# Optimization experiments

Hardware: AMD Instinct MI355X
Metric: run time of the kernel (lower is better)

## Reference

```python
import jax, jax.numpy as jnp
import numpy as np

B, N, OUTERDIM, DIM, N_CLASSES = 2, 6000, 1024, 512, 2
HEADS, DIM_HEAD, INNER = 8, 64, 512
LANDMARKS, PINV_ITERS, KPAD = 256, 6, 16  # residual conv kernel 33 -> pad 16
SCALE = DIM_HEAD ** -0.5


def layer_norm(x, g, b, eps=1e-5):
    mu = x.mean(-1, keepdims=True)
    var = jnp.var(x, axis=-1, keepdims=True)
    return (x - mu) * jax.lax.rsqrt(var + eps) * g + b


def moore_penrose_pinv(x, iters=PINV_ITERS):
    # x: [b, h, m, m]
    abs_x = jnp.abs(x)
    col = abs_x.sum(-1)
    row = abs_x.sum(-2)
    z = jnp.swapaxes(x, -1, -2) / (jnp.max(col) * jnp.max(row))
    I = jnp.eye(x.shape[-1], dtype=x.dtype)
    for _ in range(iters):
        xz = x @ z
        z = 0.25 * z @ (13 * I - xz @ (15 * I - xz @ (7 * I - xz)))
    return z


def nystrom_attention(x, w_qkv, w_out, b_out, conv_w):
    b, n, _ = x.shape
    pad = (-n) % LANDMARKS
    xp = jnp.pad(x, ((0, 0), (pad, 0), (0, 0)))  # pad at FRONT, as in lucidrains impl
    npad = n + pad
    qkv = xp @ w_qkv.T  # [b, npad, 3*inner]
    q, k, v = [t.reshape(b, npad, HEADS, DIM_HEAD).transpose(0, 2, 1, 3)
               for t in jnp.split(qkv, 3, axis=-1)]
    q = q * SCALE
    l = npad // LANDMARKS  # tokens per landmark
    q_l = q.reshape(b, HEADS, LANDMARKS, l, DIM_HEAD).sum(3) / l
    k_l = k.reshape(b, HEADS, LANDMARKS, l, DIM_HEAD).sum(3) / l
    attn1 = jax.nn.softmax(jnp.einsum('bhid,bhjd->bhij', q, k_l), axis=-1)   # [b,h,npad,m]
    attn2 = jax.nn.softmax(jnp.einsum('bhid,bhjd->bhij', q_l, k_l), axis=-1)  # [b,h,m,m]
    attn3 = jax.nn.softmax(jnp.einsum('bhid,bhjd->bhij', q_l, k), axis=-1)    # [b,h,m,npad]
    out = (attn1 @ moore_penrose_pinv(attn2)) @ (attn3 @ v)  # [b,h,npad,d]
    # depthwise residual conv over sequence dim (per head), kernel (33,1)
    out = out + jax.lax.conv_general_dilated(
        v, conv_w, window_strides=(1, 1), padding=((KPAD, KPAD), (0, 0)),
        dimension_numbers=('NCHW', 'OIHW', 'NCHW'), feature_group_count=HEADS)
    out = out.transpose(0, 2, 1, 3).reshape(b, npad, INNER)
    out = out @ w_out.T + b_out
    return out[:, -n:]


def setup_inputs() -> dict:
    key = jax.random.key(0)
    ks = jax.random.split(key, 12)
    w = lambda k, shape: 0.02 * jax.random.normal(k, shape, dtype=jnp.float32)
    inp = {
        'data': jax.random.normal(ks[0], (B, N, OUTERDIM), dtype=jnp.float32),
        'w1': w(ks[1], (DIM, OUTERDIM)), 'b1': jnp.zeros((DIM,), jnp.float32),
        'cls_token': jax.random.normal(ks[2], (1, 1, DIM), dtype=jnp.float32),
        'ln1_g': jnp.ones((DIM,), jnp.float32), 'ln1_b': jnp.zeros((DIM,), jnp.float32),
        'qkv1_w': w(ks[3], (3 * INNER, DIM)),
        'out1_w': w(ks[4], (DIM, INNER)), 'out1_b': jnp.zeros((DIM,), jnp.float32),
        'conv1_w': w(ks[5], (HEADS, 1, 33, 1)),
        'ln2_g': jnp.ones((DIM,), jnp.float32), 'ln2_b': jnp.zeros((DIM,), jnp.float32),
        'qkv2_w': w(ks[6], (3 * INNER, DIM)),
        'out2_w': w(ks[7], (DIM, INNER)), 'out2_b': jnp.zeros((DIM,), jnp.float32),
        'conv2_w': w(ks[8], (HEADS, 1, 33, 1)),
        'lnf_g': jnp.ones((DIM,), jnp.float32), 'lnf_b': jnp.zeros((DIM,), jnp.float32),
        'w2': w(ks[9], (N_CLASSES, DIM)), 'b2': jnp.zeros((N_CLASSES,), jnp.float32),
    }
    return inp


def reference(data, w1, b1, cls_token, ln1_g, ln1_b, qkv1_w, out1_w, out1_b, conv1_w,
              ln2_g, ln2_b, qkv2_w, out2_w, out2_b, conv2_w, lnf_g, lnf_b, w2, b2):
    h = jax.nn.relu(data @ w1.T + b1)  # [B, N, DIM]
    H = h.shape[1]
    side = int(np.ceil(np.sqrt(H)))
    add = side * side - H
    h = jnp.concatenate([h, h[:, :add]], axis=1)  # square padding: 6084
    cls = jnp.broadcast_to(cls_token, (h.shape[0], 1, h.shape[2]))
    h = jnp.concatenate([cls, h], axis=1)  # +CLS: 6085
    h = h + nystrom_attention(layer_norm(h, ln1_g, ln1_b), qkv1_w, out1_w, out1_b, conv1_w)
    h = h + nystrom_attention(layer_norm(h, ln2_g, ln2_b), qkv2_w, out2_w, out2_b, conv2_w)
    h = layer_norm(h, lnf_g, lnf_b)[:, 0]
    logits = h @ w2.T + b2
    return logits
```

## Files before the change

### kernel.cpp

```cpp
#include <hip/hip_runtime.h>
#include <cstdint>
#include <cstddef>

namespace {

constexpr int DIMC  = 512;
constexpr int SEQ   = 6085;
constexpr int NPAD  = 6144;
constexpr int PADF  = 59;
constexpr int LMK   = 256;
constexpr int BHN   = 16;
constexpr int KSPL  = 16;
constexpr int MPADR = 6016;

typedef __attribute__((ext_vector_type(8))) short bf8_t;
typedef __attribute__((ext_vector_type(4))) float f4_t;

#define MFMA(a, b, c) __builtin_amdgcn_mfma_f32_16x16x32_bf16(a, b, c, 0, 0, 0)

#define SWZB(r, cu) (((((r) << 6) + ((cu) << 1))) ^ (((r) & 7) << 4))

#define GLDS16(gp, lp) __builtin_amdgcn_global_load_lds( \
    (const __attribute__((address_space(1))) void*)(gp), \
    (__attribute__((address_space(3))) void*)(lp), 16, 0, 0)

__device__ __forceinline__ ushort f2bf(float f) {
    union { float f; uint32_t u; } c{f};
    uint32_t u = c.u;
    return (ushort)((u + 0x7FFFu + ((u >> 16) & 1u)) >> 16);
}
__device__ __forceinline__ float bf2f(ushort u) {
    union { uint32_t u; float f; } c{(uint32_t)u << 16};
    return c.f;
}

__device__ __forceinline__ float waveSum(float v) {
#pragma unroll
    for (int o = 32; o > 0; o >>= 1) v += __shfl_xor(v, o, 64);
    return v;
}
__device__ __forceinline__ float waveMax(float v) {
#pragma unroll
    for (int o = 32; o > 0; o >>= 1) v = fmaxf(v, __shfl_xor(v, o, 64));
    return v;
}
__device__ __forceinline__ float blockSum256(float v, float* sm) {
    v = waveSum(v);
    __syncthreads();
    if ((threadIdx.x & 63) == 0) sm[threadIdx.x >> 6] = v;
    __syncthreads();
    return sm[0] + sm[1] + sm[2] + sm[3];
}
__device__ __forceinline__ float blockMax256(float v, float* sm) {
    v = waveMax(v);
    __syncthreads();
    if ((threadIdx.x & 63) == 0) sm[threadIdx.x >> 6] = v;
    __syncthreads();
    return fmaxf(fmaxf(sm[0], sm[1]), fmaxf(sm[2], sm[3]));
}
__device__ __forceinline__ float grpMax(float v) {
    v = fmaxf(v, __shfl_xor(v, 1, 64));
    v = fmaxf(v, __shfl_xor(v, 2, 64));
    v = fmaxf(v, __shfl_xor(v, 4, 64));
    v = fmaxf(v, __shfl_xor(v, 8, 64));
    return v;
}
__device__ __forceinline__ float grpSum(float v) {
    v += __shfl_xor(v, 1, 64);
    v += __shfl_xor(v, 2, 64);
    v += __shfl_xor(v, 4, 64);
    v += __shfl_xor(v, 8, 64);
    return v;
}

template<int EPI>
__global__ __launch_bounds__(256)
void gemm_bt(const ushort* __restrict__ A, const ushort* __restrict__ B,
             void* __restrict__ Cv, int M, int N, int K,
             int lda, int ldb, int ldc,
             long long sA, long long sB, long long sC,
             const float* __restrict__ bias, int relu,
             ushort* __restrict__ qp, ushort* __restrict__ kp, ushort* __restrict__ vp)
{
    __shared__ __align__(16) char As_s[128 * 128];
    __shared__ __align__(16) char Bs_s[128 * 128];
    const int gx = gridDim.x, gy = gridDim.y;
    const int total = gx * gy * gridDim.z;
    int flat = (blockIdx.z * gy + blockIdx.y) * gx + blockIdx.x;
    {
        int q = total >> 3, r = total & 7;
        int xcd = flat & 7, idx = flat >> 3;
        flat = (xcd < r ? xcd * (q + 1) : r * (q + 1) + (xcd - r) * q) + idx;
    }
    const int z = flat / (gx * gy);
    const int rem = flat - z * gx * gy;
    const int by = rem / gx, bx = rem - by * gx;

    const ushort* Ab = A + (size_t)z * sA;
    const ushort* Bb = B + (size_t)z * sB;
    const int row0 = by * 128, col0 = bx * 128;
    const int tid = threadIdx.x, wid = tid >> 6, lane = tid & 63;
    const int wr = wid >> 1, wc = wid & 1, lr = lane & 15, kg = lane >> 4;
    const int srow = lane >> 3, sq = lane & 7;
    f4_t acc[4][4] = {};
    for (int k0 = 0; k0 < K; k0 += 64) {
        __syncthreads();
#pragma unroll
        for (int i = 0; i < 4; ++i) {
            int r = wid * 32 + i * 8 + srow;
            int qs = sq ^ (r & 7);
            GLDS16(Ab + (size_t)(row0 + r) * lda + k0 + qs * 8,
                   As_s + (wid * 32 + i * 8) * 128);
        }
#pragma unroll
        for (int i = 0; i < 4; ++i) {
            int r = wid * 32 + i * 8 + srow;
            int qs = sq ^ (r & 7);
            GLDS16(Bb + (size_t)(col0 + r) * ldb + k0 + qs * 8,
                   Bs_s + (wid * 32 + i * 8) * 128);
        }
        asm volatile("s_waitcnt vmcnt(0)" ::: "memory");
        __syncthreads();
#pragma unroll
        for (int ks = 0; ks < 2; ++ks) {
            bf8_t af[4], bg[4];
#pragma unroll
            for (int mr = 0; mr < 4; ++mr) {
                int r = wr * 64 + mr * 16 + lr;
                af[mr] = *(const bf8_t*)(As_s + r * 128 + ((((ks << 2) | kg) ^ (r & 7)) << 4));
            }
#pragma unroll
            for (int nr = 0; nr < 4; ++nr) {
                int r = wc * 64 + nr * 16 + lr;
                bg[nr] = *(const bf8_t*)(Bs_s + r * 128 + ((((ks << 2) | kg) ^ (r & 7)) << 4));
            }
#pragma unroll
            for (int mr = 0; mr < 4; ++mr)
#pragma unroll
                for (int nr = 0; nr < 4; ++nr)
                    acc[mr][nr] = MFMA(af[mr], bg[nr], acc[mr][nr]);
        }
    }
#pragma unroll
    for (int mr = 0; mr < 4; ++mr) {
#pragma unroll
        for (int nr = 0; nr < 4; ++nr) {
#pragma unroll
            for (int r = 0; r < 4; ++r) {
                int gm = row0 + wr * 64 + mr * 16 + kg * 4 + r;
                int gn = col0 + wc * 64 + nr * 16 + lr;
                if (gm >= M || gn >= N) continue;
                float val = acc[mr][nr][r];
                if (EPI == 0) {
                    if (bias) val += bias[gn];
                    if (relu) val = fmaxf(val, 0.f);
                    ((float*)Cv)[(size_t)z * sC + (size_t)gm * ldc + gn] = val;
                } else if (EPI == 1) {
                    ((ushort*)Cv)[(size_t)z * sC + (size_t)gm * ldc + gn] = f2bf(val);
                } else {
                    int b = (gm >= NPAD) ? 1 : 0;
                    int i = gm - b * NPAD;
                    int which = gn >> 9, hh = (gn >> 6) & 7, d = gn & 63;
                    int bh = b * 8 + hh;
                    if (which == 0)
                        qp[((size_t)bh * NPAD + i) * 64 + d] = f2bf(val * 0.125f);
                    else if (which == 1)
                        kp[((size_t)bh * NPAD + i) * 64 + d] = f2bf(val);
                    else
                        vp[((size_t)bh * NPAD + i) * 64 + d] = f2bf(val);
                }
            }
        }
    }
}

__global__ __launch_bounds__(256)
void gemm_ns(const ushort* __restrict__ A, const ushort* __restrict__ B,
             ushort* __restrict__ C, ushort* __restrict__ C2, ushort* __restrict__ CT,
             float alpha, float c2d, int K, int N,
             long long sA, long long sB, long long sC, long long sCT)
{
    __shared__ __align__(16) char As_s[64 * 64];
    __shared__ __align__(16) char Bs_s[64 * 64];
    const int z = blockIdx.z;
    const int row0 = blockIdx.y * 64, col0 = blockIdx.x * 64;
    const int tid = threadIdx.x;
    const int wid = tid >> 6, lane = tid & 63;
    const int lr = lane & 15, kg = lane >> 4;
    const ushort* Ab = A + (size_t)z * sA;
    const ushort* Bb = B + (size_t)z * sB;
    f4_t acc[4] = {};
    const int am = tid >> 2, ac8 = (tid & 3) * 8;
    for (int k0 = 0; k0 < K; k0 += 32) {
        *(bf8_t*)(As_s + SWZB(am, ac8)) = *(const bf8_t*)&Ab[(size_t)(row0 + am) * K + k0 + ac8];
#pragma unroll
        for (int p = 0; p < 8; ++p) {
            int kk = p * 4 + (tid >> 6), n = tid & 63;
            *(ushort*)(Bs_s + SWZB(n, kk)) = Bb[(size_t)(k0 + kk) * N + col0 + n];
        }
        __syncthreads();
        bf8_t af = *(const bf8_t*)(As_s + SWZB(wid * 16 + lr, kg * 8));
#pragma unroll
        for (int j = 0; j < 4; ++j) {
            bf8_t bg = *(const bf8_t*)(Bs_s + SWZB(j * 16 + lr, kg * 8));
            acc[j] = MFMA(af, bg, acc[j]);
        }
        __syncthreads();
    }
#pragma unroll
    for (int j = 0; j < 4; ++j) {
#pragma unroll
        for (int r = 0; r < 4; ++r) {
            int gm = row0 + wid * 16 + kg * 4 + r;
            int gn = col0 + j * 16 + lr;
            float val = alpha * acc[j][r];
            if (C)  C[(size_t)z * sC + (size_t)gm * N + gn] = f2bf(val);
            if (C2) C2[(size_t)z * sC + (size_t)gm * N + gn] = f2bf(((gm == gn) ? c2d : 0.f) - val);
            if (CT) CT[(size_t)z * sCT + (size_t)gn * LMK + gm] = f2bf(val);
        }
    }
}

__global__ __launch_bounds__(256)
void pv_splitk(const ushort* __restrict__ S, const ushort* __restrict__ v,
               float* __restrict__ o2p)
{
    __shared__ __align__(16) char As_s[128 * 64];
    __shared__ __align__(16) char Bs_s[64 * 64];
    const int split = blockIdx.x, mt = blockIdx.y, bh = blockIdx.z;
    const int tid = threadIdx.x;
    const int wid = tid >> 6, lane = tid & 63;
    const int lr = lane & 15, kg = lane >> 4;
    const ushort* Sb = S + (size_t)bh * LMK * NPAD + (size_t)(mt * 128) * NPAD;
    const ushort* vb = v + (size_t)bh * NPAD * 64;
    const int ks0 = split * (NPAD / KSPL);
    f4_t acc[2][4] = {};
    for (int k0 = ks0; k0 < ks0 + NPAD / KSPL; k0 += 32) {
#pragma unroll
        for (int p = 0; p < 2; ++p) {
            int idx = p * 256 + tid;
            int m = idx >> 2, kc = (idx & 3) * 8;
            *(bf8_t*)(As_s + SWZB(m, kc)) = *(const bf8_t*)&Sb[(size_t)m * NPAD + k0 + kc];
        }
#pragma unroll
        for (int p = 0; p < 8; ++p) {
            int kk = p * 4 + (tid >> 6), n = tid & 63;
            *(ushort*)(Bs_s + SWZB(n, kk)) = vb[(size_t)(k0 + kk) * 64 + n];
        }
        __syncthreads();
        bf8_t af[2], bg[4];
#pragma unroll
        for (int i = 0; i < 2; ++i)
            af[i] = *(const bf8_t*)(As_s + SWZB(wid * 32 + i * 16 + lr, kg * 8));
#pragma unroll
        for (int j = 0; j < 4; ++j)
            bg[j] = *(const bf8_t*)(Bs_s + SWZB(j * 16 + lr, kg * 8));
#pragma unroll
        for (int i = 0; i < 2; ++i)
#pragma unroll
            for (int j = 0; j < 4; ++j)
                acc[i][j] = MFMA(af[i], bg[j], acc[i][j]);
        __syncthreads();
    }
#pragma unroll
    for (int i = 0; i < 2; ++i)
#pragma unroll
        for (int j = 0; j < 4; ++j)
#pragma unroll
            for (int r = 0; r < 4; ++r) {
                int gm = mt * 128 + wid * 32 + i * 16 + kg * 4 + r;
                int gn = j * 16 + lr;
                o2p[((size_t)(split * BHN + bh) * LMK + gm) * 64 + gn] = acc[i][j][r];
            }
}

__global__ void reduce_o2(const float* __restrict__ o2p, ushort* __restrict__ o2) {
    int idx = blockIdx.x * 256 + threadIdx.x;
    int bh = idx >> 14, e = idx & 16383;
    float s = 0.f;
#pragma unroll
    for (int sp = 0; sp < KSPL; ++sp)
        s += o2p[((size_t)(sp * BHN + bh) << 14) + e];
    o2[idx] = f2bf(s);
}

__global__ __launch_bounds__(256)
void attn1_fused(const ushort* __restrict__ q, const ushort* __restrict__ kl,
                 const ushort* __restrict__ Wt, ushort* __restrict__ ot)
{
    __shared__ __align__(16) char P_s[64 * 512];
    const int mt = blockIdx.x;
    const int bh = blockIdx.y;
    const int b = bh >> 3, hh = bh & 7;
    const int tid = threadIdx.x, wid = tid >> 6, lane = tid & 63;
    const int lr = lane & 15, kg = lane >> 4;
    const int row0 = mt * 64, rowb = wid * 16;
    const ushort* qb  = q  + (size_t)bh * NPAD * 64;
    const ushort* klb = kl + (size_t)bh * LMK * 64;
    const ushort* Wtb = Wt + (size_t)bh * 128 * 256;

    f4_t acc[16];
#pragma unroll
    for (int nf = 0; nf < 16; ++nf) acc[nf] = (f4_t){0.f, 0.f, 0.f, 0.f};
#pragma unroll
    for (int ks = 0; ks < 2; ++ks) {
        bf8_t af = *(const bf8_t*)&qb[(size_t)(row0 + rowb + lr) * 64 + ks * 32 + kg * 8];
#pragma unroll
        for (int nf = 0; nf < 16; ++nf) {
            bf8_t bg = *(const bf8_t*)&klb[(size_t)(nf * 16 + lr) * 64 + ks * 32 + kg * 8];
            acc[nf] = MFMA(af, bg, acc[nf]);
        }
    }
    float inv_s[4];
    {
        float mx[4] = {-3.0e38f, -3.0e38f, -3.0e38f, -3.0e38f};
#pragma unroll
        for (int nf = 0; nf < 16; ++nf)
#pragma unroll
            for (int r = 0; r < 4; ++r) mx[r] = fmaxf(mx[r], acc[nf][r]);
#pragma unroll
        for (int r = 0; r < 4; ++r) mx[r] = grpMax(mx[r]);
        float sum[4] = {0.f, 0.f, 0.f, 0.f};
        const int rb2 = rowb + kg * 4;
        const int cc2 = (lr & 7) * 2, chi = lr >> 3;
#pragma unroll
        for (int nf = 0; nf < 16; ++nf)
#pragma unroll
            for (int r = 0; r < 4; ++r) {
                float e = __expf(acc[nf][r] - mx[r]);
                sum[r] += e;
                int row = rb2 + r;
                int chunk = (2 * nf + chi) ^ (row & 7);
                *(ushort*)(P_s + row * 512 + chunk * 16 + cc2) = f2bf(e);
            }
#pragma unroll
        for (int r = 0; r < 4; ++r) inv_s[r] = 1.f / grpSum(sum[r]);
    }
    f4_t acc2[4] = {};
#pragma unroll
    for (int kt = 0; kt < 8; ++kt) {
        int row = rowb + lr;
        int chunk = (kt * 4 + kg) ^ (row & 7);
        bf8_t af2 = *(const bf8_t*)(P_s + row * 512 + chunk * 16);
#pragma unroll
        for (int nf = 0; nf < 4; ++nf) {
            bf8_t bg = *(const bf8_t*)&Wtb[(size_t)(nf * 16 + lr) * 256 + kt * 32 + kg * 8];
            acc2[nf] = MFMA(af2, bg, acc2[nf]);
        }
    }
#pragma unroll
    for (int nf = 0; nf < 4; ++nf)
#pragma unroll
        for (int r = 0; r < 4; ++r) {
            int gm = row0 + rowb + kg * 4 + r;
            int gn = nf * 16 + lr;
            ot[((size_t)(b * NPAD + gm)) * DIMC + hh * 64 + gn] = f2bf(acc2[nf][r] * inv_s[r]);
        }
}

__global__ void cvt_bf16(const float* __restrict__ in, ushort* __restrict__ out, int n8) {
    int i = blockIdx.x * 256 + threadIdx.x;
    if (i >= n8) return;
    float4 a = ((const float4*)in)[i * 2], b = ((const float4*)in)[i * 2 + 1];
    ushort4 lo = { f2bf(a.x), f2bf(a.y), f2bf(a.z), f2bf(a.w) };
    ushort4 hi = { f2bf(b.x), f2bf(b.y), f2bf(b.z), f2bf(b.w) };
    ((ushort4*)out)[i * 2] = lo;
    ((ushort4*)out)[i * 2 + 1] = hi;
}

__global__ void extend_h(float* __restrict__ h, const float* __restrict__ cls) {
    int b = blockIdx.y, bx = blockIdx.x;
    float* hb = h + (size_t)b * SEQ * DIMC;
    for (int c = threadIdx.x; c < DIMC; c += 256) {
        if (bx == 0) hb[c] = cls[c];
        else hb[(size_t)(6000 + bx) * DIMC + c] = hb[(size_t)bx * DIMC + c];
    }
}

__global__ void zero_xp_pad(ushort* __restrict__ xp) {
    int e = blockIdx.x * 256 + threadIdx.x;
    int b = e / (PADF * DIMC);
    int rest = e - b * (PADF * DIMC);
    xp[(size_t)b * NPAD * DIMC + rest] = 0;
}

__global__ __launch_bounds__(128)
void ln_to_xp(const float* __restrict__ h, const float* __restrict__ g,
              const float* __restrict__ bb, ushort* __restrict__ xp)
{
    __shared__ float sm[2];
    int r = blockIdx.x;
    int b = r / SEQ, i = r - b * SEQ;
    int t = threadIdx.x;
    const float4* row = (const float4*)(h + (size_t)r * DIMC);
    float4 x = row[t];
    float s  = x.x + x.y + x.z + x.w;
    float sq = x.x * x.x + x.y * x.y + x.z * x.z + x.w * x.w;
    s = waveSum(s);
    sq = waveSum(sq);
    int w = t >> 6;
    if ((t & 63) == 0) sm[w] = s;
    __syncthreads();
    float S = sm[0] + sm[1];
    __syncthreads();
    if ((t & 63) == 0) sm[w] = sq;
    __syncthreads();
    float SQ = sm[0] + sm[1];
    float mu = S * (1.f / DIMC);
    float var = SQ * (1.f / DIMC) - mu * mu;
    float rs = rsqrtf(var + 1e-5f);
    float4 gg = ((const float4*)g)[t];
    float4 bv = ((const float4*)bb)[t];
    ushort4 o;
    o.x = f2bf((x.x - mu) * rs * gg.x + bv.x);
    o.y = f2bf((x.y - mu) * rs * gg.y + bv.y);
    o.z = f2bf((x.z - mu) * rs * gg.z + bv.z);
    o.w = f2bf((x.w - mu) * rs * gg.w + bv.w);
    ((ushort4*)(xp + ((size_t)b * NPAD + PADF + i) * DIMC))[t] = o;
}

__global__ void landmark_mean(const ushort* __restrict__ in, ushort* __restrict__ out) {
    int m = blockIdx.x, bh = blockIdx.y, d = threadIdx.x;
    const ushort* p = in + ((size_t)bh * NPAD + (size_t)m * (NPAD / LMK)) * 64 + d;
    float s = 0.f;
#pragma unroll
    for (int j = 0; j < NPAD / LMK; ++j) s += bf2f(p[(size_t)j * 64]);
    out[((size_t)bh * LMK + m) * 64 + d] = f2bf(s * (1.f / (NPAD / LMK)));
}

__global__ __launch_bounds__(256)
void softmax_bf_wide(ushort* __restrict__ S) {
    __shared__ float sm[4];
    ushort* p = S + (size_t)blockIdx.x * NPAD;
    int t = threadIdx.x;
    float v[24];
    float mx = -1e30f;
#pragma unroll
    for (int j = 0; j < 24; ++j) { v[j] = bf2f(p[j * 256 + t]); mx = fmaxf(mx, v[j]); }
    float bm = blockMax256(mx, sm);
    float s = 0.f;
#pragma unroll
    for (int j = 0; j < 24; ++j) { v[j] = __expf(v[j] - bm); s += v[j]; }
    float bs = blockSum256(s, sm);
    float inv = 1.f / bs;
#pragma unroll
    for (int j = 0; j < 24; ++j) p[j * 256 + t] = f2bf(v[j] * inv);
}

__global__ __launch_bounds__(256)
void softmax_bf256(ushort* __restrict__ S) {
    __shared__ float sm[4];
    ushort* p = S + (size_t)blockIdx.x * 256;
    int t = threadIdx.x;
    float v = bf2f(p[t]);
    float bm = blockMax256(v, sm);
    float e = __expf(v - bm);
    float bs = blockSum256(e, sm);
    p[t] = f2bf(e / bs);
}

__global__ __launch_bounds__(256)
void colsum_max(const ushort* __restrict__ X, float* __restrict__ scal) {
    __shared__ float sm[4];
    int bh = blockIdx.x, t = threadIdx.x;
    const ushort* Xb = X + ((size_t)bh << 16);
    float s = 0.f;
#pragma unroll 8
    for (int i = 0; i < 256; ++i) s += bf2f(Xb[(size_t)i * 256 + t]);
    float m = blockMax256(s, sm);
    if (t == 0) atomicMax((unsigned int*)scal, __float_as_uint(m));
}

__global__ void init_z(const ushort* __restrict__ X, const float* __restrict__ scal,
                       ushort* __restrict__ Z) {
    size_t e = (size_t)blockIdx.x * 256 + threadIdx.x;
    int c = (int)(e & 255);
    int r = (int)((e >> 8) & 255);
    size_t bh = e >> 16;
    float inv = 1.f / scal[0];
    Z[e] = f2bf(bf2f(X[(bh << 16) + (size_t)c * 256 + r]) * inv);
}

__global__ __launch_bounds__(256)
void conv_add(const ushort* __restrict__ v, const float* __restrict__ cw,
              ushort* __restrict__ ot)
{
    __shared__ float w[33];
    __shared__ ushort vt[96][64];
    int bh = blockIdx.y;
    int b = bh >> 3, hh = bh & 7;
    int i0 = blockIdx.x * 64;
    int t = threadIdx.x;
    if (t < 33) w[t] = cw[hh * 33 + t];
    const ushort* vb = v + (size_t)bh * NPAD * 64;
    int d = t & 63;
    for (int rr = t >> 6; rr < 96; rr += 4) {
        int j = i0 - 16 + rr;
        vt[rr][d] = (j >= 0 && j < NPAD) ? vb[(size_t)j * 64 + d] : (ushort)0;
    }
    __syncthreads();
    for (int ii = t >> 6; ii < 64; ii += 4) {
        float acc = 0.f;
#pragma unroll
        for (int kk = 0; kk < 33; ++kk) acc += w[kk] * bf2f(vt[ii + kk][d]);
        size_t off = ((size_t)(b * NPAD + i0 + ii)) * DIMC + hh * 64 + d;
        ot[off] = f2bf(bf2f(ot[off]) + acc);
    }
}

__global__ void residual_add(float* __restrict__ h, const float* __restrict__ y) {
    size_t e = (size_t)blockIdx.x * 256 + threadIdx.x;
    int c = (int)(e & 511);
    size_t ri = e >> 9;
    int i = (int)(ri % SEQ);
    int b = (int)(ri / SEQ);
    h[e] += y[((size_t)b * NPAD + PADF + i) * DIMC + c];
}

__global__ __launch_bounds__(256)
void final_head(const float* __restrict__ h, const float* __restrict__ g,
                const float* __restrict__ bb, const float* __restrict__ w2,
                const float* __restrict__ b2, float* __restrict__ out)
{
    __shared__ float row[DIMC];
    __shared__ float sm[4];
    int b = blockIdx.x;
    int t = threadIdx.x;
    const float* x = h + (size_t)b * SEQ * DIMC;
    float v0 = x[t], v1 = x[t + 256];
    float S = blockSum256(v0 + v1, sm);
    float SQ = blockSum256(v0 * v0 + v1 * v1, sm);
    float mu = S * (1.f / DIMC);
    float rs = rsqrtf(SQ * (1.f / DIMC) - mu * mu + 1e-5f);
    row[t] = (v0 - mu) * rs * g[t] + bb[t];
    row[t + 256] = (v1 - mu) * rs * g[t + 256] + bb[t + 256];
    __syncthreads();
    if (t < 64) {
        float a0 = 0.f, a1 = 0.f;
        for (int idx = t; idx < DIMC; idx += 64) {
            a0 += row[idx] * w2[idx];
            a1 += row[idx] * w2[DIMC + idx];
        }
        a0 = waveSum(a0);
        a1 = waveSum(a1);
        if (t == 0) {
            out[b * 2 + 0] = a0 + b2[0];
            out[b * 2 + 1] = a1 + b2[1];
        }
    }
}

void bt(int epi, const ushort* A, const ushort* B, void* C, int M, int N, int K,
        int lda, int ldb, int ldc, long long sA, long long sB, long long sC, int batch,
        const float* bias, int relu, ushort* qp, ushort* kp, ushort* vp, hipStream_t s)
{
    dim3 g((N + 127) / 128, (M + 127) / 128, batch), blk(256);
    switch (epi) {
    case 0: gemm_bt<0><<<g, blk, 0, s>>>(A, B, C, M, N, K, lda, ldb, ldc, sA, sB, sC, bias, relu, qp, kp, vp); break;
    case 1: gemm_bt<1><<<g, blk, 0, s>>>(A, B, C, M, N, K, lda, ldb, ldc, sA, sB, sC, bias, relu, qp, kp, vp); break;
    default: gemm_bt<2><<<g, blk, 0, s>>>(A, B, C, M, N, K, lda, ldb, ldc, sA, sB, sC, bias, relu, qp, kp, vp); break;
    }
}

void ns(const ushort* A, const ushort* B, ushort* C, ushort* C2, ushort* CT,
        float alpha, float c2d, int M, int N, int K,
        long long sA, long long sB, long long sC, long long sCT, hipStream_t s)
{
    dim3 g(N / 64, M / 64, BHN), blk(256);
    gemm_ns<<<g, blk, 0, s>>>(A, B, C, C2, CT, alpha, c2d, K, N, sA, sB, sC, sCT);
}

struct WS {
    float *h, *scal, *o2p, *y;
    ushort *xp, *q, *k, *v, *ql, *kl;
    ushort *datab, *w1b, *qkvwb1, *qkvwb2, *outwb1, *outwb2;
    ushort *X, *Z0, *Z1, *XZ, *TA, *TB, *TC;
    ushort *o2b, *Wt, *S, *ot;
};

void nystrom_layer(float* h, const float* lng, const float* lnb,
                   const ushort* qkvwb, const ushort* outwb, const float* outb,
                   const float* convw, const WS& w, hipStream_t s)
{
    const long long SM = (long long)LMK * LMK;
    zero_xp_pad<<<(2 * PADF * DIMC) / 256, 256, 0, s>>>(w.xp);
    ln_to_xp<<<2 * SEQ, 128, 0, s>>>(h, lng, lnb, w.xp);
    bt(2, w.xp, qkvwb, nullptr, 2 * NPAD, 3 * DIMC, DIMC, DIMC, DIMC, 0,
       0, 0, 0, 1, nullptr, 0, w.q, w.k, w.v, s);
    landmark_mean<<<dim3(LMK, BHN), 64, 0, s>>>(w.q, w.ql);
    landmark_mean<<<dim3(LMK, BHN), 64, 0, s>>>(w.k, w.kl);
    bt(1, w.ql, w.kl, w.X, LMK, LMK, 64, 64, 64, LMK,
       (long long)LMK * 64, (long long)LMK * 64, SM, BHN,
       nullptr, 0, nullptr, nullptr, nullptr, s);
    softmax_bf256<<<BHN * LMK, 256, 0, s>>>(w.X);
    hipMemsetAsync(w.scal, 0, 8, s);
    colsum_max<<<BHN, 256, 0, s>>>(w.X, w.scal);
    init_z<<<(BHN * LMK * LMK) / 256, 256, 0, s>>>(w.X, w.scal, w.Z0);
    ushort* Zc = w.Z0;
    ushort* Zn = w.Z1;
    for (int it = 0; it < 6; ++it) {
        ns(w.X, Zc, w.XZ, w.TA, nullptr, 1.f, 7.f, LMK, LMK, LMK, SM, SM, SM, 0, s);
        ns(w.XZ, w.TA, w.TB, w.TC, nullptr, 1.f, 15.f, LMK, LMK, LMK, SM, SM, SM, 0, s);
        ns(w.XZ, w.TC, w.TB, w.TA, nullptr, 1.f, 13.f, LMK, LMK, LMK, SM, SM, SM, 0, s);
        ns(Zc, w.TA, Zn, nullptr, nullptr, 0.25f, 0.f, LMK, LMK, LMK, SM, SM, SM, 0, s);
        ushort* t = Zc; Zc = Zn; Zn = t;
    }
    bt(1, w.ql, w.k, w.S, LMK, NPAD, 64, 64, 64, NPAD,
       (long long)LMK * 64, (long long)NPAD * 64, (long long)LMK * NPAD, BHN,
       nullptr, 0, nullptr, nullptr, nullptr, s);
    softmax_bf_wide<<<BHN * LMK, 256, 0, s>>>(w.S);
    pv_splitk<<<dim3(KSPL, 2, BHN), 256, 0, s>>>(w.S, w.v, w.o2p);
    reduce_o2<<<BHN * LMK * 64 / 256, 256, 0, s>>>(w.o2p, w.o2b);
    ns(Zc, w.o2b, nullptr, nullptr, w.Wt, 1.f, 0.f, LMK, 64, LMK,
       SM, (long long)LMK * 64, 0, 128 * 256, s);
    attn1_fused<<<dim3(NPAD / 64, BHN), 256, 0, s>>>(w.q, w.kl, w.Wt, w.ot);
    conv_add<<<dim3(NPAD / 64, BHN), 256, 0, s>>>(w.v, convw, w.ot);
    bt(0, w.ot, outwb, w.y, 2 * NPAD, DIMC, DIMC, DIMC, DIMC, DIMC,
       0, 0, 0, 1, outb, 0, nullptr, nullptr, nullptr, s);
    residual_add<<<(2 * SEQ * DIMC) / 256, 256, 0, s>>>(h, w.y);
}

}

extern "C" void kernel_launch(void* const* d_in, const int* in_sizes, int n_in,
                              void* d_out, int out_size, void* d_ws, size_t ws_size,
                              hipStream_t stream)
{
    (void)in_sizes; (void)n_in; (void)out_size;
    const float* data  = (const float*)d_in[0];
    const float* w1    = (const float*)d_in[1];
    const float* b1    = (const float*)d_in[2];
    const float* cls   = (const float*)d_in[3];
    const float* ln1g  = (const float*)d_in[4];
    const float* ln1b  = (const float*)d_in[5];
    const float* qkv1w = (const float*)d_in[6];
    const float* out1w = (const float*)d_in[7];
    const float* out1b = (const float*)d_in[8];
    const float* conv1 = (const float*)d_in[9];
    const float* ln2g  = (const float*)d_in[10];
    const float* ln2b  = (const float*)d_in[11];
    const float* qkv2w = (const float*)d_in[12];
    const float* out2w = (const float*)d_in[13];
    const float* out2b = (const float*)d_in[14];
    const float* conv2 = (const float*)d_in[15];
    const float* lnfg  = (const float*)d_in[16];
    const float* lnfb  = (const float*)d_in[17];
    const float* w2    = (const float*)d_in[18];
    const float* b2    = (const float*)d_in[19];
    float* out = (float*)d_out;

    if (ws_size < 209473792ull) return;
    char* p = (char*)d_ws;
    auto alloc = [&](size_t bytes) { char* r = p; p += (bytes + 255) & ~(size_t)255; return r; };
    WS w;
    w.h     = (float*)alloc((size_t)2 * SEQ * DIMC * 4);
    w.xp    = (ushort*)alloc((size_t)2 * NPAD * DIMC * 2);
    w.q     = (ushort*)alloc((size_t)BHN * NPAD * 64 * 2);
    w.k     = (ushort*)alloc((size_t)BHN * NPAD * 64 * 2);
    w.v     = (ushort*)alloc((size_t)BHN * NPAD * 64 * 2);
    w.ql    = (ushort*)alloc((size_t)BHN * LMK * 64 * 2);
    w.kl    = (ushort*)alloc((size_t)BHN * LMK * 64 * 2);
    w.scal  = (float*)alloc(256);
    w.datab = (ushort*)alloc((size_t)2 * MPADR * 1024 * 2);
    w.w1b   = (ushort*)alloc((size_t)512 * 1024 * 2);
    w.qkvwb1= (ushort*)alloc((size_t)1536 * 512 * 2);
    w.qkvwb2= (ushort*)alloc((size_t)1536 * 512 * 2);
    w.outwb1= (ushort*)alloc((size_t)512 * 512 * 2);
    w.outwb2= (ushort*)alloc((size_t)512 * 512 * 2);
    w.X     = (ushort*)alloc((size_t)BHN * LMK * LMK * 2);
    w.Z0    = (ushort*)alloc((size_t)BHN * LMK * LMK * 2);
    w.Z1    = (ushort*)alloc((size_t)BHN * LMK * LMK * 2);
    w.XZ    = (ushort*)alloc((size_t)BHN * LMK * LMK * 2);
    w.TA    = (ushort*)alloc((size_t)BHN * LMK * LMK * 2);
    w.TB    = (ushort*)alloc((size_t)BHN * LMK * LMK * 2);
    w.TC    = (ushort*)alloc((size_t)BHN * LMK * LMK * 2);
    w.o2p   = (float*)alloc((size_t)KSPL * BHN * LMK * 64 * 4);
    w.o2b   = (ushort*)alloc((size_t)BHN * LMK * 64 * 2);
    w.Wt    = (ushort*)alloc((size_t)BHN * 128 * 256 * 2);
    w.S     = (ushort*)alloc((size_t)BHN * LMK * NPAD * 2);
    w.y     = (float*)w.S;
    w.ot    = w.k;

    for (int b = 0; b < 2; ++b)
        cvt_bf16<<<3000, 256, 0, stream>>>(data + (size_t)b * 6000 * 1024,
                                           w.datab + (size_t)b * MPADR * 1024, 768000);
    cvt_bf16<<<256, 256, 0, stream>>>(w1, w.w1b, 65536);
    cvt_bf16<<<384, 256, 0, stream>>>(qkv1w, w.qkvwb1, 98304);
    cvt_bf16<<<384, 256, 0, stream>>>(qkv2w, w.qkvwb2, 98304);
    cvt_bf16<<<128, 256, 0, stream>>>(out1w, w.outwb1, 32768);
    cvt_bf16<<<128, 256, 0, stream>>>(out2w, w.outwb2, 32768);

    bt(0, w.datab, w.w1b, w.h + DIMC, 6000, DIMC, 1024, 1024, 1024, DIMC,
       (long long)MPADR * 1024, 0, (long long)SEQ * DIMC, 2, b1, 1,
       nullptr, nullptr, nullptr, stream);
    extend_h<<<dim3(85, 2), 256, 0, stream>>>(w.h, cls);

    nystrom_layer(w.h, ln1g, ln1b, w.qkvwb1, w.outwb1, out1b, conv1, w, stream);
    nystrom_layer(w.h, ln2g, ln2b, w.qkvwb2, w.outwb2, out2b, conv2, w, stream);

    final_head<<<2, 256, 0, stream>>>(w.h, lnfg, lnfb, w2, b2, out);
}
```

Measured before the change: 1.017 ms.

## Switch Newton-Schulz pinv GEMMs to NT layout with transposed operand buffers

Replaces the NN batched GEMM used by the pseudo-inverse iterations with an NT GEMM, so B tiles load as 16-byte vectors instead of strided 2-byte scalar loads. Each step now writes its results transposed, Z keeps both a normal and a transposed copy, and reduce_o2 writes o2 transposed. Output flags become template parameters, so the epilogue carries no runtime branches. The cost is extra transposed (strided) stores and more workspace buffers.

```diff
diff --git a/kernel.cpp b/kernel.cpp
--- a/kernel.cpp
+++ b/kernel.cpp
@@ -174,30 +174,26 @@
     }
 }
 
-__global__ __launch_bounds__(256)
-void gemm_ns(const ushort* __restrict__ A, const ushort* __restrict__ B,
-             ushort* __restrict__ C, ushort* __restrict__ C2, ushort* __restrict__ CT,
-             float alpha, float c2d, int K, int N,
-             long long sA, long long sB, long long sC, long long sCT)
+template<int OC, int OCT, int CTD>
+__global__ __launch_bounds__(256)
+void gemm_nt(const ushort* __restrict__ A, const ushort* __restrict__ Bt,
+             ushort* __restrict__ C, ushort* __restrict__ CT,
+             float alpha, float cd, int K, int ldC, int ldCT,
+             long long sA, long long sBt, long long sC, long long sCT)
 {
     __shared__ __align__(16) char As_s[64 * 64];
     __shared__ __align__(16) char Bs_s[64 * 64];
     const int z = blockIdx.z;
     const int row0 = blockIdx.y * 64, col0 = blockIdx.x * 64;
-    const int tid = threadIdx.x;
-    const int wid = tid >> 6, lane = tid & 63;
+    const int tid = threadIdx.x, wid = tid >> 6, lane = tid & 63;
     const int lr = lane & 15, kg = lane >> 4;
     const ushort* Ab = A + (size_t)z * sA;
-    const ushort* Bb = B + (size_t)z * sB;
+    const ushort* Bb = Bt + (size_t)z * sBt;
+    const int sr = tid >> 2, sc = (tid & 3) * 8;
     f4_t acc[4] = {};
-    const int am = tid >> 2, ac8 = (tid & 3) * 8;
     for (int k0 = 0; k0 < K; k0 += 32) {
-        *(bf8_t*)(As_s + SWZB(am, ac8)) = *(const bf8_t*)&Ab[(size_t)(row0 + am) * K + k0 + ac8];
-#pragma unroll
-        for (int p = 0; p < 8; ++p) {
-            int kk = p * 4 + (tid >> 6), n = tid & 63;
-            *(ushort*)(Bs_s + SWZB(n, kk)) = Bb[(size_t)(k0 + kk) * N + col0 + n];
-        }
+        *(bf8_t*)(As_s + SWZB(sr, sc)) = *(const bf8_t*)&Ab[(size_t)(row0 + sr) * K + k0 + sc];
+        *(bf8_t*)(Bs_s + SWZB(sr, sc)) = *(const bf8_t*)&Bb[(size_t)(col0 + sr) * K + k0 + sc];
         __syncthreads();
         bf8_t af = *(const bf8_t*)(As_s + SWZB(wid * 16 + lr, kg * 8));
 #pragma unroll
@@ -214,9 +210,9 @@
             int gm = row0 + wid * 16 + kg * 4 + r;
             int gn = col0 + j * 16 + lr;
             float val = alpha * acc[j][r];
-            if (C)  C[(size_t)z * sC + (size_t)gm * N + gn] = f2bf(val);
-            if (C2) C2[(size_t)z * sC + (size_t)gm * N + gn] = f2bf(((gm == gn) ? c2d : 0.f) - val);
-            if (CT) CT[(size_t)z * sCT + (size_t)gn * LMK + gm] = f2bf(val);
+            if (OC) C[(size_t)z * sC + (size_t)gm * ldC + gn] = f2bf(val);
+            if (OCT) CT[(size_t)z * sCT + (size_t)gn * ldCT + gm] =
+                f2bf(CTD ? (((gm == gn) ? cd : 0.f) - val) : val);
         }
     }
 }
@@ -274,14 +270,14 @@
             }
 }
 
-__global__ void reduce_o2(const float* __restrict__ o2p, ushort* __restrict__ o2) {
+__global__ void reduce_o2(const float* __restrict__ o2p, ushort* __restrict__ o2t) {
     int idx = blockIdx.x * 256 + threadIdx.x;
-    int bh = idx >> 14, e = idx & 16383;
+    int bh = idx >> 14, m = (idx >> 6) & 255, d = idx & 63;
     float s = 0.f;
 #pragma unroll
     for (int sp = 0; sp < KSPL; ++sp)
-        s += o2p[((size_t)(sp * BHN + bh) << 14) + e];
-    o2[idx] = f2bf(s);
+        s += o2p[((size_t)(sp * BHN + bh) << 14) + (m << 6) + d];
+    o2t[((size_t)bh * 64 + d) * 256 + m] = f2bf(s);
 }
 
 __global__ __launch_bounds__(256)
@@ -472,13 +468,14 @@
 }
 
 __global__ void init_z(const ushort* __restrict__ X, const float* __restrict__ scal,
-                       ushort* __restrict__ Z) {
+                       ushort* __restrict__ Z, ushort* __restrict__ Zt) {
     size_t e = (size_t)blockIdx.x * 256 + threadIdx.x;
     int c = (int)(e & 255);
     int r = (int)((e >> 8) & 255);
     size_t bh = e >> 16;
     float inv = 1.f / scal[0];
-    Z[e] = f2bf(bf2f(X[(bh << 16) + (size_t)c * 256 + r]) * inv);
+    Z[e]  = f2bf(bf2f(X[(bh << 16) + (size_t)c * 256 + r]) * inv);
+    Zt[e] = f2bf(bf2f(X[e]) * inv);
 }
 
 __global__ __launch_bounds__(256)
@@ -562,20 +559,25 @@
     }
 }
 
-void ns(const ushort* A, const ushort* B, ushort* C, ushort* C2, ushort* CT,
-        float alpha, float c2d, int M, int N, int K,
-        long long sA, long long sB, long long sC, long long sCT, hipStream_t s)
+void nt(int mode, const ushort* A, const ushort* Bt, ushort* C, ushort* CT,
+        float alpha, float cd, int M, int N, int K, int ldC, int ldCT,
+        long long sA, long long sBt, long long sC, long long sCT, hipStream_t s)
 {
     dim3 g(N / 64, M / 64, BHN), blk(256);
-    gemm_ns<<<g, blk, 0, s>>>(A, B, C, C2, CT, alpha, c2d, K, N, sA, sB, sC, sCT);
+    switch (mode) {
+    case 0: gemm_nt<1, 1, 1><<<g, blk, 0, s>>>(A, Bt, C, CT, alpha, cd, K, ldC, ldCT, sA, sBt, sC, sCT); break;
+    case 1: gemm_nt<0, 1, 1><<<g, blk, 0, s>>>(A, Bt, C, CT, alpha, cd, K, ldC, ldCT, sA, sBt, sC, sCT); break;
+    case 2: gemm_nt<1, 1, 0><<<g, blk, 0, s>>>(A, Bt, C, CT, alpha, cd, K, ldC, ldCT, sA, sBt, sC, sCT); break;
+    default: gemm_nt<0, 1, 0><<<g, blk, 0, s>>>(A, Bt, C, CT, alpha, cd, K, ldC, ldCT, sA, sBt, sC, sCT); break;
+    }
 }
 
 struct WS {
     float *h, *scal, *o2p, *y;
     ushort *xp, *q, *k, *v, *ql, *kl;
     ushort *datab, *w1b, *qkvwb1, *qkvwb2, *outwb1, *outwb2;
-    ushort *X, *Z0, *Z1, *XZ, *TA, *TB, *TC;
-    ushort *o2b, *Wt, *S, *ot;
+    ushort *X, *Y, *TAt, *TBt, *Z0, *Z0t, *Z1, *Z1t;
+    ushort *o2t, *Wt, *S, *ot;
 };
 
 void nystrom_layer(float* h, const float* lng, const float* lnb,
@@ -595,24 +597,25 @@
     softmax_bf256<<<BHN * LMK, 256, 0, s>>>(w.X);
     hipMemsetAsync(w.scal, 0, 8, s);
     colsum_max<<<BHN, 256, 0, s>>>(w.X, w.scal);
-    init_z<<<(BHN * LMK * LMK) / 256, 256, 0, s>>>(w.X, w.scal, w.Z0);
-    ushort* Zc = w.Z0;
-    ushort* Zn = w.Z1;
+    init_z<<<(BHN * LMK * LMK) / 256, 256, 0, s>>>(w.X, w.scal, w.Z0, w.Z0t);
+    ushort *Zc = w.Z0, *Zct = w.Z0t, *Zn = w.Z1, *Znt = w.Z1t;
     for (int it = 0; it < 6; ++it) {
-        ns(w.X, Zc, w.XZ, w.TA, nullptr, 1.f, 7.f, LMK, LMK, LMK, SM, SM, SM, 0, s);
-        ns(w.XZ, w.TA, w.TB, w.TC, nullptr, 1.f, 15.f, LMK, LMK, LMK, SM, SM, SM, 0, s);
-        ns(w.XZ, w.TC, w.TB, w.TA, nullptr, 1.f, 13.f, LMK, LMK, LMK, SM, SM, SM, 0, s);
-        ns(Zc, w.TA, Zn, nullptr, nullptr, 0.25f, 0.f, LMK, LMK, LMK, SM, SM, SM, 0, s);
-        ushort* t = Zc; Zc = Zn; Zn = t;
+        nt(0, w.X, Zct, w.Y, w.TAt, 1.f, 7.f, LMK, LMK, LMK, 256, 256, SM, SM, SM, SM, s);
+        nt(1, w.Y, w.TAt, nullptr, w.TBt, 1.f, 15.f, LMK, LMK, LMK, 256, 256, SM, SM, 0, SM, s);
+        nt(1, w.Y, w.TBt, nullptr, w.TAt, 1.f, 13.f, LMK, LMK, LMK, 256, 256, SM, SM, 0, SM, s);
+        nt(2, Zc, w.TAt, Zn, Znt, 0.25f, 0.f, LMK, LMK, LMK, 256, 256, SM, SM, SM, SM, s);
+        ushort* t;
+        t = Zc; Zc = Zn; Zn = t;
+        t = Zct; Zct = Znt; Znt = t;
     }
     bt(1, w.ql, w.k, w.S, LMK, NPAD, 64, 64, 64, NPAD,
        (long long)LMK * 64, (long long)NPAD * 64, (long long)LMK * NPAD, BHN,
        nullptr, 0, nullptr, nullptr, nullptr, s);
     softmax_bf_wide<<<BHN * LMK, 256, 0, s>>>(w.S);
     pv_splitk<<<dim3(KSPL, 2, BHN), 256, 0, s>>>(w.S, w.v, w.o2p);
-    reduce_o2<<<BHN * LMK * 64 / 256, 256, 0, s>>>(w.o2p, w.o2b);
-    ns(Zc, w.o2b, nullptr, nullptr, w.Wt, 1.f, 0.f, LMK, 64, LMK,
-       SM, (long long)LMK * 64, 0, 128 * 256, s);
+    reduce_o2<<<BHN * LMK * 64 / 256, 256, 0, s>>>(w.o2p, w.o2t);
+    nt(3, Zc, w.o2t, nullptr, w.Wt, 1.f, 0.f, LMK, 64, LMK, 256, 256,
+       SM, 64 * 256, 0, 128 * 256, s);
     attn1_fused<<<dim3(NPAD / 64, BHN), 256, 0, s>>>(w.q, w.kl, w.Wt, w.ot);
     conv_add<<<dim3(NPAD / 64, BHN), 256, 0, s>>>(w.v, convw, w.ot);
     bt(0, w.ot, outwb, w.y, 2 * NPAD, DIMC, DIMC, DIMC, DIMC, DIMC,
@@ -668,14 +671,15 @@
     w.outwb1= (ushort*)alloc((size_t)512 * 512 * 2);
     w.outwb2= (ushort*)alloc((size_t)512 * 512 * 2);
     w.X     = (ushort*)alloc((size_t)BHN * LMK * LMK * 2);
+    w.Y     = (ushort*)alloc((size_t)BHN * LMK * LMK * 2);
+    w.TAt   = (ushort*)alloc((size_t)BHN * LMK * LMK * 2);
+    w.TBt   = (ushort*)alloc((size_t)BHN * LMK * LMK * 2);
     w.Z0    = (ushort*)alloc((size_t)BHN * LMK * LMK * 2);
+    w.Z0t   = (ushort*)alloc((size_t)BHN * LMK * LMK * 2);
     w.Z1    = (ushort*)alloc((size_t)BHN * LMK * LMK * 2);
-    w.XZ    = (ushort*)alloc((size_t)BHN * LMK * LMK * 2);
-    w.TA    = (ushort*)alloc((size_t)BHN * LMK * LMK * 2);
-    w.TB    = (ushort*)alloc((size_t)BHN * LMK * LMK * 2);
-    w.TC    = (ushort*)alloc((size_t)BHN * LMK * LMK * 2);
+    w.Z1t   = (ushort*)alloc((size_t)BHN * LMK * LMK * 2);
     w.o2p   = (float*)alloc((size_t)KSPL * BHN * LMK * 64 * 4);
-    w.o2b   = (ushort*)alloc((size_t)BHN * LMK * 64 * 2);
+    w.o2t   = (ushort*)alloc((size_t)BHN * 64 * 256 * 2);
     w.Wt    = (ushort*)alloc((size_t)BHN * 128 * 256 * 2);
     w.S     = (ushort*)alloc((size_t)BHN * LMK * NPAD * 2);
     w.y     = (float*)w.S;
```

Result: faster. 961.1 us (-5.5%).
